# Performance work log

Measured on AMD Instinct MI355X. Metric: run time of the kernel, lower is better.

## Reference

```python
import jax, jax.numpy as jnp
import numpy as np

HIDDEN = 512


def _lstm(x, kernel, rec, bias):
    # x: [B,T,D]; Keras gate order i,f,c(g),o
    xz = jnp.einsum('btd,dk->btk', x, kernel) + bias  # [B,T,4H]
    B = x.shape[0]
    init = (jnp.zeros((B, HIDDEN), x.dtype), jnp.zeros((B, HIDDEN), x.dtype))

    def step(carry, z_t):
        h, c = carry
        z = z_t + h @ rec
        i, f, g, o = jnp.split(z, 4, axis=-1)
        c = jax.nn.sigmoid(f) * c + jax.nn.sigmoid(i) * jnp.tanh(g)
        h = jax.nn.sigmoid(o) * jnp.tanh(c)
        return (h, c), h

    _, hs = jax.lax.scan(step, init, jnp.swapaxes(xz, 0, 1))
    return jnp.swapaxes(hs, 0, 1)  # [B,T,H]


def _bilstm(x, kf, rf, bf, kb, rb, bb):
    fwd = _lstm(x, kf, rf, bf)
    bwd = _lstm(x[:, ::-1], kb, rb, bb)[:, ::-1]
    return jnp.concatenate([fwd, bwd], axis=-1)  # [B,T,2H]


def _crf_nll(logits, tags, seq_lens, trans):
    # logits [B,T,N], tags [B,T] int, seq_lens [B] int, trans [N,N]
    B, T, N = logits.shape
    t_idx = jnp.arange(T)
    mask = (t_idx[None, :] < seq_lens[:, None])  # [B,T] bool
    maskf = mask.astype(logits.dtype)

    # gold sequence score: unary + pairwise transitions
    unary = jnp.take_along_axis(logits, tags[..., None], axis=-1)[..., 0]  # [B,T]
    unary_score = jnp.sum(unary * maskf, axis=-1)
    pair_maskf = maskf[:, 1:]  # pair (t-1,t) valid iff t < len
    binary = trans[tags[:, :-1], tags[:, 1:]]  # [B,T-1]
    binary_score = jnp.sum(binary * pair_maskf, axis=-1)

    # log-partition via forward algorithm (masked scan)
    alpha0 = logits[:, 0]  # [B,N]

    def step(alpha, inp):
        logit_t, valid = inp
        new = jax.nn.logsumexp(alpha[:, :, None] + trans[None], axis=1) + logit_t
        return jnp.where(valid[:, None], new, alpha), None

    xs = (jnp.swapaxes(logits[:, 1:], 0, 1), jnp.swapaxes(mask[:, 1:], 0, 1))
    alpha, _ = jax.lax.scan(step, alpha0, xs)
    log_z = jax.nn.logsumexp(alpha, axis=-1)  # [B]
    return -(unary_score + binary_score - log_z)


def setup_inputs() -> dict:
    key = jax.random.key(0)
    ks = jax.random.split(key, 12)
    B, T, D, H, N = 32, 256, 768, HIDDEN, 25
    s_in = 1.0 / np.sqrt(D)
    s_rec = 1.0 / np.sqrt(H)
    return {
        'embeddings': jax.random.normal(ks[0], (B, T, D), jnp.float32),
        'targets': jax.random.randint(ks[1], (B, T), 0, N, jnp.int32),
        'seq_lens': jax.random.randint(ks[2], (B,), 1, T + 1, jnp.int32),
        'k_fwd': jax.random.normal(ks[3], (D, 4 * H), jnp.float32) * s_in,
        'r_fwd': jax.random.normal(ks[4], (H, 4 * H), jnp.float32) * s_rec,
        'b_fwd': jnp.zeros((4 * H,), jnp.float32),
        'k_bwd': jax.random.normal(ks[5], (D, 4 * H), jnp.float32) * s_in,
        'r_bwd': jax.random.normal(ks[6], (H, 4 * H), jnp.float32) * s_rec,
        'b_bwd': jnp.zeros((4 * H,), jnp.float32),
        'dense_w': jax.random.normal(ks[7], (2 * H, N), jnp.float32) / np.sqrt(2 * H),
        'dense_b': jnp.zeros((N,), jnp.float32),
        'transitions': jax.random.uniform(ks[8], (N, N), jnp.float32),
    }


def reference(embeddings, targets, seq_lens, k_fwd, r_fwd, b_fwd,
              k_bwd, r_bwd, b_bwd, dense_w, dense_b, transitions):
    seq_lens = jnp.clip(seq_lens, 1, embeddings.shape[1])
    h = _bilstm(embeddings, k_fwd, r_fwd, b_fwd, k_bwd, r_bwd, b_bwd)
    logits = jax.nn.selu(jnp.einsum('bth,hn->btn', h, dense_w) + dense_b)
    nll = _crf_nll(logits, targets, seq_lens, transitions)  # [B]
    loss = jnp.mean(nll)
    return loss, logits
```

## Files before the change

kernel.cpp:

```cpp
#include <hip/hip_runtime.h>
#include <hip/hip_bf16.h>
#include <math.h>

#define HID 512
#define GATES 2048
#define BT 8192
#define TT 256
#define BB 32
#define DIN 768
#define NTAG 25
#define UPB 4
#define NBLK 128
#define FSTR 4
#define EREP 8
#define ESTR 16

typedef _Float16 half2v __attribute__((ext_vector_type(2)));
typedef _Float16 half8  __attribute__((ext_vector_type(8)));
typedef float    f32x4  __attribute__((ext_vector_type(4)));

__device__ __forceinline__ half2v pack2h(float a, float b) {
  return __builtin_bit_cast(half2v, __builtin_amdgcn_cvt_pkrtz(a, b));
}

__device__ __forceinline__ float sigf(float x) { return 1.f / (1.f + __expf(-x)); }

__device__ __forceinline__ void gld_lds16(const void* g, void* l) {
  __builtin_amdgcn_global_load_lds(
      (const __attribute__((address_space(1))) unsigned int*)g,
      (__attribute__((address_space(3))) unsigned int*)l, 16, 0, 0);
}

__global__ __launch_bounds__(256) void prep_all(
    const float* __restrict__ emb, unsigned short* __restrict__ emb16,
    const float* __restrict__ Kf, const float* __restrict__ Kb,
    unsigned short* __restrict__ KTf, unsigned short* __restrict__ KTb,
    const float* __restrict__ W, unsigned short* __restrict__ WT16)
{
  __shared__ float tile[64][65];
  const int bid = blockIdx.x;
  const int tid = threadIdx.x;

  if (bid < 1024) {
    const int m = bid * 8 + (tid >> 5);
    const int c0 = tid & 31;
    #pragma unroll
    for (int p = 0; p < 3; ++p) {
      const int c = c0 + p * 32;
      const int kb = c >> 3, s = c & 7;
      const float* src = emb + (size_t)m * DIN + c * 8;
      const float4 v0 = *(const float4*)src;
      const float4 v1 = *(const float4*)(src + 4);
      half8 hv;
      hv[0] = (_Float16)v0.x; hv[1] = (_Float16)v0.y;
      hv[2] = (_Float16)v0.z; hv[3] = (_Float16)v0.w;
      hv[4] = (_Float16)v1.x; hv[5] = (_Float16)v1.y;
      hv[6] = (_Float16)v1.z; hv[7] = (_Float16)v1.w;
      *(half8*)(emb16 + (size_t)m * DIN + kb * 64 + (s ^ (m & 7)) * 8) = hv;
    }
  } else if (bid < 1792) {
    const int r = bid - 1024;
    const int dir = r / 384;
    const int r2 = r % 384;
    const int k0 = (r2 >> 5) * 64;
    const int n0 = (r2 & 31) * 64;
    const float* __restrict__ K = dir ? Kb : Kf;
    unsigned short* __restrict__ KT = dir ? KTb : KTf;
    #pragma unroll
    for (int p = 0; p < 4; ++p) {
      const int idx = p * 256 + tid;
      const int kr = idx >> 4, c4 = (idx & 15) * 4;
      const float4 v = *(const float4*)(K + (size_t)(k0 + kr) * GATES + n0 + c4);
      tile[kr][c4 + 0] = v.x; tile[kr][c4 + 1] = v.y;
      tile[kr][c4 + 2] = v.z; tile[kr][c4 + 3] = v.w;
    }
    __syncthreads();
    #pragma unroll
    for (int p = 0; p < 2; ++p) {
      const int idx = p * 256 + tid;
      const int nr = idx >> 3, s = idx & 7;
      half8 hv;
      #pragma unroll
      for (int x = 0; x < 8; ++x) hv[x] = (_Float16)tile[s * 8 + x][nr];
      *(half8*)(KT + (size_t)(n0 + nr) * DIN + k0 + (s ^ (nr & 7)) * 8) = hv;
    }
  } else {
    for (int id = tid; id < 32 * 1024; id += 256) {
      const int n = id >> 10, k = id & 1023;
      const float v = (n < NTAG) ? W[(size_t)k * NTAG + n] : 0.f;
      ((_Float16*)WT16)[id] = (_Float16)v;
    }
  }
}

__global__ __launch_bounds__(256) void gemm_xz(
    const unsigned short* __restrict__ emb16,
    const unsigned short* __restrict__ KTf, const unsigned short* __restrict__ KTb,
    const float* __restrict__ bf, const float* __restrict__ bb,
    float* __restrict__ xzf, float* __restrict__ xzb)
{
  const int dir = blockIdx.z;
  const unsigned short* __restrict__ KT = dir ? KTb : KTf;
  const float* __restrict__ bias = dir ? bb : bf;
  float* __restrict__ C = dir ? xzb : xzf;
  const int n0 = blockIdx.x * 128;
  const int m0 = blockIdx.y * 128;

  __shared__ __align__(16) char A_lds[128 * 64 * 2];
  __shared__ __align__(16) char B_lds[128 * 64 * 2];

  const int tid = threadIdx.x;
  const int lane = tid & 63, wid = tid >> 6;
  const int wm = wid >> 1, wn = wid & 1;
  const int lm = lane & 15, lk = lane >> 4;

  f32x4 acc[4][4];
  #pragma unroll
  for (int i = 0; i < 4; ++i)
    #pragma unroll
    for (int j = 0; j < 4; ++j) acc[i][j] = (f32x4){0.f, 0.f, 0.f, 0.f};

  for (int kt = 0; kt < DIN / 64; ++kt) {
    __syncthreads();
    #pragma unroll
    for (int i = 0; i < 4; ++i) {
      const int g = wid * 256 + i * 64 + lane;
      const int r = g >> 3, s = g & 7;
      gld_lds16(emb16 + (size_t)(m0 + r) * DIN + (kt * 8 + s) * 8,
                A_lds + (size_t)(wid * 256 + i * 64) * 16);
      gld_lds16(KT + (size_t)(n0 + r) * DIN + (kt * 8 + s) * 8,
                B_lds + (size_t)(wid * 256 + i * 64) * 16);
    }
    __syncthreads();

    #pragma unroll
    for (int kh = 0; kh < 2; ++kh) {
      half8 a[4], b[4];
      #pragma unroll
      for (int mt = 0; mt < 4; ++mt) {
        const int rloc = wm * 64 + mt * 16 + lm;
        const int kslot = kh * 4 + lk;
        a[mt] = *(const half8*)(A_lds + rloc * 128 + ((kslot ^ (rloc & 7)) << 4));
      }
      #pragma unroll
      for (int nt = 0; nt < 4; ++nt) {
        const int nloc = wn * 64 + nt * 16 + lm;
        const int kslot = kh * 4 + lk;
        b[nt] = *(const half8*)(B_lds + nloc * 128 + ((kslot ^ (nloc & 7)) << 4));
      }
      #pragma unroll
      for (int mt = 0; mt < 4; ++mt)
        #pragma unroll
        for (int nt = 0; nt < 4; ++nt)
          acc[mt][nt] = __builtin_amdgcn_mfma_f32_16x16x32_f16(a[mt], b[nt], acc[mt][nt], 0, 0, 0);
    }
  }

  #pragma unroll
  for (int nt = 0; nt < 4; ++nt) {
    const int col = n0 + wn * 64 + nt * 16 + lm;
    const float bs = bias[col];
    #pragma unroll
    for (int mt = 0; mt < 4; ++mt) {
      const int rowb = m0 + wm * 64 + mt * 16 + lk * 4;
      const f32x4 v = acc[mt][nt];
      #pragma unroll
      for (int g = 0; g < 4; ++g)
        C[(size_t)(rowb + g) * GATES + col] = v[g] + bs;
    }
  }
}

__global__ __launch_bounds__(256, 1) void lstm_persist(
    const float* __restrict__ xzf, const float* __restrict__ xzb,
    const float* __restrict__ Rf, const float* __restrict__ Rb,
    unsigned int* __restrict__ hGf, unsigned int* __restrict__ hGb,
    int* __restrict__ flg,
    int* __restrict__ ep)
{
  const int bid = blockIdx.x;
  const int dir = bid & 1;
  const int blk = bid >> 1;
  const int u0 = blk * UPB;
  const int tid = threadIdx.x;
  const int c = tid & 15;
  const int j = (c & 3) * HID + u0 + (c >> 2);
  const int lane = tid & 63, w = tid >> 6;
  const int lm = lane & 15, lk = lane >> 4;

  const float* __restrict__ R  = dir ? Rb : Rf;
  const float* __restrict__ xz = dir ? xzb : xzf;
  unsigned int* __restrict__ hGd = dir ? hGb : hGf;
  int* __restrict__ flgd = flg + (size_t)dir * TT * NBLK * FSTR;
  int* __restrict__ epd  = ep  + (size_t)dir * TT * EREP * ESTR;

  __shared__ uint4 hs4[BB * 65];
  __shared__ float redm[4][BB][18];
  __shared__ float zbuf[BB][20];

  half8 Rbf[4];
  #pragma unroll
  for (int kti = 0; kti < 4; ++kti) {
    const int kb = (w * 4 + kti) * 32 + lk * 8;
    half8 hv;
    #pragma unroll
    for (int x = 0; x < 8; ++x) hv[x] = (_Float16)R[(size_t)(kb + x) * GATES + j];
    Rbf[kti] = hv;
  }

  float cst = 0.f;
  const int b_o = tid & 31, u_o = tid >> 5;
  const int fb0 = tid >> 4, fb1 = (tid >> 4) + 16;
  const bool leader = (blk == 0);

  for (int s = 0; s < TT; ++s) {
    const int t = dir ? (TT - 1 - s) : s;

    const float x0 = xz[((size_t)fb0 * TT + t) * GATES + j];
    const float x1 = xz[((size_t)fb1 * TT + t) * GATES + j];

    if (s > 0) {
      const int tprev = dir ? t + 1 : t - 1;
      if (leader) {
        if (tid < NBLK) {
          while (!__hip_atomic_load(&flgd[((s - 1) * NBLK + tid) * FSTR],
                                    __ATOMIC_RELAXED, __HIP_MEMORY_SCOPE_AGENT))
            __builtin_amdgcn_s_sleep(1);
        }
        __syncthreads();
        if (tid < EREP)
          __hip_atomic_store(&epd[((s - 1) * EREP + tid) * ESTR], 1,
                             __ATOMIC_RELAXED, __HIP_MEMORY_SCOPE_AGENT);
      } else {
        if (tid == 0) {
          while (!__hip_atomic_load(&epd[((s - 1) * EREP + (blk & 7)) * ESTR],
                                    __ATOMIC_RELAXED, __HIP_MEMORY_SCOPE_AGENT))
            __builtin_amdgcn_s_sleep(1);
        }
        __syncthreads();
      }
      const uint4* hsrc = (const uint4*)(hGd + (size_t)tprev * BB * 256);
      #pragma unroll
      for (int it = 0; it < 8; ++it) {
        const int g4 = tid + it * 256;
        const uint4 v = hsrc[g4];
        hs4[(g4 >> 6) * 65 + (g4 & 63)] = v;
      }
    } else {
      const uint4 zz = make_uint4(0u, 0u, 0u, 0u);
      #pragma unroll
      for (int it = 0; it < 9; ++it) {
        const int idx = tid + it * 256;
        if (idx < BB * 65) hs4[idx] = zz;
      }
    }
    __syncthreads();

    f32x4 acc0 = (f32x4){0.f, 0.f, 0.f, 0.f};
    f32x4 acc1 = (f32x4){0.f, 0.f, 0.f, 0.f};
    #pragma unroll
    for (int kti = 0; kti < 4; ++kti) {
      const int k4 = (w * 4 + kti) * 4 + lk;
      const half8 a0 = *(const half8*)&hs4[(lm) * 65 + k4];
      const half8 a1 = *(const half8*)&hs4[(16 + lm) * 65 + k4];
      acc0 = __builtin_amdgcn_mfma_f32_16x16x32_f16(a0, Rbf[kti], acc0, 0, 0, 0);
      acc1 = __builtin_amdgcn_mfma_f32_16x16x32_f16(a1, Rbf[kti], acc1, 0, 0, 0);
    }
    #pragma unroll
    for (int g = 0; g < 4; ++g) {
      redm[w][lk * 4 + g][lm] = acc0[g];
      redm[w][16 + lk * 4 + g][lm] = acc1[g];
    }
    __syncthreads();

    {
      const float za = redm[0][fb0][c] + redm[1][fb0][c] + redm[2][fb0][c] + redm[3][fb0][c] + x0;
      const float zb2 = redm[0][fb1][c] + redm[1][fb1][c] + redm[2][fb1][c] + redm[3][fb1][c] + x1;
      zbuf[fb0][c] = za;
      zbuf[fb1][c] = zb2;
    }
    __syncthreads();

    if (tid < 128) {
      const float zi = zbuf[b_o][u_o * 4 + 0];
      const float zf = zbuf[b_o][u_o * 4 + 1];
      const float zg = zbuf[b_o][u_o * 4 + 2];
      const float zo = zbuf[b_o][u_o * 4 + 3];
      cst = sigf(zf) * cst + sigf(zi) * tanhf(zg);
      const float h = sigf(zo) * tanhf(cst);
      const float hp2 = __shfl_xor(h, 32);
      if ((tid & 32) == 0) {
        const half2v p = pack2h(h, hp2);
        __hip_atomic_store(&hGd[((size_t)t * BB + b_o) * 256 + blk * 2 + (u_o >> 1)],
                           __builtin_bit_cast(unsigned int, p),
                           __ATOMIC_RELAXED, __HIP_MEMORY_SCOPE_AGENT);
      }
    }
    __syncthreads();
    if (tid == 0)
      __hip_atomic_store(&flgd[(s * NBLK + blk) * FSTR], 1, __ATOMIC_RELAXED,
                         __HIP_MEMORY_SCOPE_AGENT);
  }
}

__global__ __launch_bounds__(256) void dense_selu(
    const unsigned int* __restrict__ hGf, const unsigned int* __restrict__ hGb,
    const unsigned short* __restrict__ WT16, const float* __restrict__ bias,
    float* __restrict__ out)
{
  const int q0 = blockIdx.x * 128;
  __shared__ __align__(16) char A_lds[128 * 64 * 2];
  __shared__ __align__(16) char B_lds[32 * 64 * 2];

  const int tid = threadIdx.x;
  const int lane = tid & 63, w = tid >> 6;
  const int lm = lane & 15, lk = lane >> 4;

  f32x4 acc[2][2];
  #pragma unroll
  for (int i = 0; i < 2; ++i)
    #pragma unroll
    for (int jj = 0; jj < 2; ++jj) acc[i][jj] = (f32x4){0.f, 0.f, 0.f, 0.f};

  for (int kt = 0; kt < 16; ++kt) {
    const int k0 = kt * 64;
    __syncthreads();
    #pragma unroll
    for (int p = 0; p < 4; ++p) {
      const int id = p * 256 + tid;
      const int r = id >> 3, s = id & 7;
      const int k = k0 + s * 8;
      const unsigned int* src = (k < 512)
          ? hGf + (size_t)(q0 + r) * 256 + (k >> 1)
          : hGb + (size_t)(q0 + r) * 256 + ((k - 512) >> 1);
      const uint4 v = *(const uint4*)src;
      *(uint4*)(A_lds + r * 128 + ((s ^ (r & 7)) << 4)) = v;
    }
    {
      const int r = tid >> 3, s = tid & 7;
      const uint4 v = *(const uint4*)(WT16 + (size_t)r * 1024 + k0 + s * 8);
      *(uint4*)(B_lds + r * 128 + ((s ^ (r & 7)) << 4)) = v;
    }
    __syncthreads();

    #pragma unroll
    for (int kh = 0; kh < 2; ++kh) {
      const int kslot = kh * 4 + lk;
      half8 a[2], b[2];
      #pragma unroll
      for (int mt = 0; mt < 2; ++mt) {
        const int rloc = w * 32 + mt * 16 + lm;
        a[mt] = *(const half8*)(A_lds + rloc * 128 + ((kslot ^ (rloc & 7)) << 4));
      }
      #pragma unroll
      for (int nt = 0; nt < 2; ++nt) {
        const int nloc = nt * 16 + lm;
        b[nt] = *(const half8*)(B_lds + nloc * 128 + ((kslot ^ (nloc & 7)) << 4));
      }
      #pragma unroll
      for (int mt = 0; mt < 2; ++mt)
        #pragma unroll
        for (int nt = 0; nt < 2; ++nt)
          acc[mt][nt] = __builtin_amdgcn_mfma_f32_16x16x32_f16(a[mt], b[nt], acc[mt][nt], 0, 0, 0);
    }
  }

  const float scale = 1.0507009873554805f, alf = 1.6732632423543772f;
  #pragma unroll
  for (int nt = 0; nt < 2; ++nt) {
    const int col = nt * 16 + lm;
    if (col < NTAG) {
      const float bs = bias[col];
      #pragma unroll
      for (int mt = 0; mt < 2; ++mt) {
        const int rowb = q0 + w * 32 + mt * 16 + lk * 4;
        const f32x4 vv = acc[mt][nt];
        #pragma unroll
        for (int g = 0; g < 4; ++g) {
          const int q = rowb + g;
          const int bt = (q & 31) * 256 + (q >> 5);
          float v = vv[g] + bs;
          v = v > 0.f ? scale * v : scale * alf * (__expf(v) - 1.f);
          out[(size_t)bt * NTAG + col] = v;
        }
      }
    }
  }
}

__global__ __launch_bounds__(64) void crf_kernel(
    const float* __restrict__ logits,
    const int* __restrict__ tags, const int* __restrict__ lens,
    const float* __restrict__ trans, float* __restrict__ nll)
{
  const int b = blockIdx.x;
  const int tid = threadIdx.x;
  __shared__ float tr[NTAG * NTAG];
  __shared__ float al[NTAG];
  __shared__ float red[2];
  for (int i = tid; i < NTAG * NTAG; i += 64) tr[i] = trans[i];
  __syncthreads();

  int len = lens[b];
  len = len < 1 ? 1 : (len > TT ? TT : len);
  const size_t base = (size_t)b * TT;

  float us = 0.f, bs = 0.f;
  for (int t = tid; t < TT; t += 64) {
    if (t < len) us += logits[(base + t) * NTAG + tags[base + t]];
    if (t >= 1 && t < len) bs += tr[tags[base + t - 1] * NTAG + tags[base + t]];
  }
  #pragma unroll
  for (int off = 32; off > 0; off >>= 1) {
    us += __shfl_down(us, off);
    bs += __shfl_down(bs, off);
  }
  if (tid == 0) { red[0] = us; red[1] = bs; }

  if (tid < NTAG) al[tid] = logits[base * NTAG + tid];
  __syncthreads();

  for (int t = 1; t < len; ++t) {
    float nv = 0.f;
    if (tid < NTAG) {
      float m = -3.4e38f;
      #pragma unroll
      for (int i = 0; i < NTAG; ++i) m = fmaxf(m, al[i] + tr[i * NTAG + tid]);
      float ss = 0.f;
      #pragma unroll
      for (int i = 0; i < NTAG; ++i) ss += __expf(al[i] + tr[i * NTAG + tid] - m);
      nv = m + __logf(ss) + logits[(base + t) * NTAG + tid];
    }
    __syncthreads();
    if (tid < NTAG) al[tid] = nv;
    __syncthreads();
  }

  if (tid == 0) {
    float m = -3.4e38f;
    for (int i = 0; i < NTAG; ++i) m = fmaxf(m, al[i]);
    float ss = 0.f;
    for (int i = 0; i < NTAG; ++i) ss += __expf(al[i] - m);
    const float logz = m + __logf(ss);
    nll[b] = -(red[0] + red[1] - logz);
  }
}

__global__ __launch_bounds__(64) void finalize(const float* __restrict__ nll, float* __restrict__ out) {
  float v = (threadIdx.x < BB) ? nll[threadIdx.x] : 0.f;
  #pragma unroll
  for (int off = 32; off > 0; off >>= 1) v += __shfl_down(v, off);
  if (threadIdx.x == 0) out[0] = v * (1.f / BB);
}

extern "C" void kernel_launch(void* const* d_in, const int* in_sizes, int n_in,
                              void* d_out, int out_size, void* d_ws, size_t ws_size,
                              hipStream_t stream) {
  const float* emb  = (const float*)d_in[0];
  const int* tags   = (const int*)d_in[1];
  const int* lens   = (const int*)d_in[2];
  const float* kf   = (const float*)d_in[3];
  const float* rf   = (const float*)d_in[4];
  const float* bf   = (const float*)d_in[5];
  const float* kb   = (const float*)d_in[6];
  const float* rb   = (const float*)d_in[7];
  const float* bb   = (const float*)d_in[8];
  const float* dw   = (const float*)d_in[9];
  const float* db   = (const float*)d_in[10];
  const float* trans= (const float*)d_in[11];
  float* out = (float*)d_out;

  float* ws  = (float*)d_ws;
  float* xzf = ws;
  float* xzb = xzf + (size_t)BT * GATES;
  unsigned int* hGf = (unsigned int*)(xzb + (size_t)BT * GATES);
  unsigned int* hGb = hGf + (size_t)TT * BB * 256;
  unsigned short* emb16 = (unsigned short*)(hGb + (size_t)TT * BB * 256);
  unsigned short* KTf = emb16 + (size_t)BT * DIN;
  unsigned short* KTb = KTf + (size_t)GATES * DIN;
  unsigned short* WT16 = KTb + (size_t)GATES * DIN;
  float* nll = (float*)(WT16 + 32 * 1024);
  int*   flg = (int*)(nll + 64);
  int*   ep  = flg + 2 * TT * NBLK * FSTR;

  (void)hipMemsetAsync(flg, 0,
                       (size_t)(2 * TT * NBLK * FSTR + 2 * TT * EREP * ESTR) * 4,
                       stream);

  prep_all<<<1793, 256, 0, stream>>>(emb, emb16, kf, kb, KTf, KTb, dw, WT16);
  gemm_xz<<<dim3(GATES / 128, BT / 128, 2), 256, 0, stream>>>(emb16, KTf, KTb, bf, bb, xzf, xzb);
  lstm_persist<<<2 * NBLK, 256, 0, stream>>>(xzf, xzb, rf, rb, hGf, hGb, flg, ep);
  dense_selu<<<BT / 128, 256, 0, stream>>>(hGf, hGb, WT16, db, out + 1);
  crf_kernel<<<32, 64, 0, stream>>>(out + 1, tags, lens, trans, nll);
  finalize<<<1, 64, 0, stream>>>(nll, out);
}
```

Measured before the change: 968.2 us.

## Store xz in fp16, give each wave a private h tile, drop block barriers

The input projection xz is now written and read as fp16, which halves the global traffic between the GEMM and the recurrent kernel. Each wave in the persistent LSTM kernel loads its own K-slice of h into a private LDS region, which removes a __syncthreads. The zbuf stage is folded into the gate computation, removing another barrier. The finalize kernel is replaced by an atomicAdd into the loss, whose zeroing happens inside dense_selu. In exchange, the gate preactivations lose precision and the order of the loss summation is no longer deterministic.

```diff
diff --git a/kernel.cpp b/kernel.cpp
--- a/kernel.cpp
+++ b/kernel.cpp
@@ -97,12 +97,12 @@
     const unsigned short* __restrict__ emb16,
     const unsigned short* __restrict__ KTf, const unsigned short* __restrict__ KTb,
     const float* __restrict__ bf, const float* __restrict__ bb,
-    float* __restrict__ xzf, float* __restrict__ xzb)
+    _Float16* __restrict__ xzf, _Float16* __restrict__ xzb)
 {
   const int dir = blockIdx.z;
   const unsigned short* __restrict__ KT = dir ? KTb : KTf;
   const float* __restrict__ bias = dir ? bb : bf;
-  float* __restrict__ C = dir ? xzb : xzf;
+  _Float16* __restrict__ C = dir ? xzb : xzf;
   const int n0 = blockIdx.x * 128;
   const int m0 = blockIdx.y * 128;
 
@@ -166,13 +166,13 @@
       const f32x4 v = acc[mt][nt];
       #pragma unroll
       for (int g = 0; g < 4; ++g)
-        C[(size_t)(rowb + g) * GATES + col] = v[g] + bs;
+        C[(size_t)(rowb + g) * GATES + col] = (_Float16)(v[g] + bs);
     }
   }
 }
 
 __global__ __launch_bounds__(256, 1) void lstm_persist(
-    const float* __restrict__ xzf, const float* __restrict__ xzb,
+    const _Float16* __restrict__ xzf, const _Float16* __restrict__ xzb,
     const float* __restrict__ Rf, const float* __restrict__ Rb,
     unsigned int* __restrict__ hGf, unsigned int* __restrict__ hGb,
     int* __restrict__ flg,
@@ -189,14 +189,13 @@
   const int lm = lane & 15, lk = lane >> 4;
 
   const float* __restrict__ R  = dir ? Rb : Rf;
-  const float* __restrict__ xz = dir ? xzb : xzf;
+  const _Float16* __restrict__ xz = dir ? xzb : xzf;
   unsigned int* __restrict__ hGd = dir ? hGb : hGf;
   int* __restrict__ flgd = flg + (size_t)dir * TT * NBLK * FSTR;
   int* __restrict__ epd  = ep  + (size_t)dir * TT * EREP * ESTR;
 
-  __shared__ uint4 hs4[BB * 65];
+  __shared__ uint4 hs4[4 * 32 * 17];
   __shared__ float redm[4][BB][18];
-  __shared__ float zbuf[BB][20];
 
   half8 Rbf[4];
   #pragma unroll
@@ -210,14 +209,19 @@
 
   float cst = 0.f;
   const int b_o = tid & 31, u_o = tid >> 5;
-  const int fb0 = tid >> 4, fb1 = (tid >> 4) + 16;
+  uint4* myhs = hs4 + w * (32 * 17);
+  const int sr = lane >> 4, si = lane & 15;
   const bool leader = (blk == 0);
 
   for (int s = 0; s < TT; ++s) {
     const int t = dir ? (TT - 1 - s) : s;
 
-    const float x0 = xz[((size_t)fb0 * TT + t) * GATES + j];
-    const float x1 = xz[((size_t)fb1 * TT + t) * GATES + j];
+    float xg[4] = {0.f, 0.f, 0.f, 0.f};
+    if (tid < 128) {
+      #pragma unroll
+      for (int g = 0; g < 4; ++g)
+        xg[g] = (float)xz[((size_t)b_o * TT + t) * GATES + g * HID + u0 + u_o];
+    }
 
     if (s > 0) {
       const int tprev = dir ? t + 1 : t - 1;
@@ -242,27 +246,25 @@
       const uint4* hsrc = (const uint4*)(hGd + (size_t)tprev * BB * 256);
       #pragma unroll
       for (int it = 0; it < 8; ++it) {
-        const int g4 = tid + it * 256;
-        const uint4 v = hsrc[g4];
-        hs4[(g4 >> 6) * 65 + (g4 & 63)] = v;
+        const int r = it * 4 + sr;
+        myhs[r * 17 + si] = hsrc[r * 64 + w * 16 + si];
       }
     } else {
       const uint4 zz = make_uint4(0u, 0u, 0u, 0u);
       #pragma unroll
-      for (int it = 0; it < 9; ++it) {
-        const int idx = tid + it * 256;
-        if (idx < BB * 65) hs4[idx] = zz;
-      }
-    }
-    __syncthreads();
+      for (int it = 0; it < 8; ++it) {
+        const int r = it * 4 + sr;
+        myhs[r * 17 + si] = zz;
+      }
+    }
 
     f32x4 acc0 = (f32x4){0.f, 0.f, 0.f, 0.f};
     f32x4 acc1 = (f32x4){0.f, 0.f, 0.f, 0.f};
     #pragma unroll
     for (int kti = 0; kti < 4; ++kti) {
-      const int k4 = (w * 4 + kti) * 4 + lk;
-      const half8 a0 = *(const half8*)&hs4[(lm) * 65 + k4];
-      const half8 a1 = *(const half8*)&hs4[(16 + lm) * 65 + k4];
+      const int cidx = kti * 4 + lk;
+      const half8 a0 = *(const half8*)&myhs[lm * 17 + cidx];
+      const half8 a1 = *(const half8*)&myhs[(16 + lm) * 17 + cidx];
       acc0 = __builtin_amdgcn_mfma_f32_16x16x32_f16(a0, Rbf[kti], acc0, 0, 0, 0);
       acc1 = __builtin_amdgcn_mfma_f32_16x16x32_f16(a1, Rbf[kti], acc1, 0, 0, 0);
     }
@@ -273,21 +275,16 @@
     }
     __syncthreads();
 
-    {
-      const float za = redm[0][fb0][c] + redm[1][fb0][c] + redm[2][fb0][c] + redm[3][fb0][c] + x0;
-      const float zb2 = redm[0][fb1][c] + redm[1][fb1][c] + redm[2][fb1][c] + redm[3][fb1][c] + x1;
-      zbuf[fb0][c] = za;
-      zbuf[fb1][c] = zb2;
-    }
-    __syncthreads();
-
     if (tid < 128) {
-      const float zi = zbuf[b_o][u_o * 4 + 0];
-      const float zf = zbuf[b_o][u_o * 4 + 1];
-      const float zg = zbuf[b_o][u_o * 4 + 2];
-      const float zo = zbuf[b_o][u_o * 4 + 3];
-      cst = sigf(zf) * cst + sigf(zi) * tanhf(zg);
-      const float h = sigf(zo) * tanhf(cst);
+      float z[4];
+      #pragma unroll
+      for (int g = 0; g < 4; ++g) {
+        const int cc = u_o * 4 + g;
+        z[g] = redm[0][b_o][cc] + redm[1][b_o][cc] + redm[2][b_o][cc] +
+               redm[3][b_o][cc] + xg[g];
+      }
+      cst = sigf(z[1]) * cst + sigf(z[0]) * tanhf(z[2]);
+      const float h = sigf(z[3]) * tanhf(cst);
       const float hp2 = __shfl_xor(h, 32);
       if ((tid & 32) == 0) {
         const half2v p = pack2h(h, hp2);
@@ -306,8 +303,9 @@
 __global__ __launch_bounds__(256) void dense_selu(
     const unsigned int* __restrict__ hGf, const unsigned int* __restrict__ hGb,
     const unsigned short* __restrict__ WT16, const float* __restrict__ bias,
-    float* __restrict__ out)
+    float* __restrict__ out, float* __restrict__ loss0)
 {
+  if (blockIdx.x == 0 && threadIdx.x == 0) *loss0 = 0.f;
   const int q0 = blockIdx.x * 128;
   __shared__ __align__(16) char A_lds[128 * 64 * 2];
   __shared__ __align__(16) char B_lds[32 * 64 * 2];
@@ -391,7 +389,7 @@
 __global__ __launch_bounds__(64) void crf_kernel(
     const float* __restrict__ logits,
     const int* __restrict__ tags, const int* __restrict__ lens,
-    const float* __restrict__ trans, float* __restrict__ nll)
+    const float* __restrict__ trans, float* __restrict__ loss0)
 {
   const int b = blockIdx.x;
   const int tid = threadIdx.x;
@@ -442,15 +440,9 @@
     float ss = 0.f;
     for (int i = 0; i < NTAG; ++i) ss += __expf(al[i] - m);
     const float logz = m + __logf(ss);
-    nll[b] = -(red[0] + red[1] - logz);
-  }
-}
-
-__global__ __launch_bounds__(64) void finalize(const float* __restrict__ nll, float* __restrict__ out) {
-  float v = (threadIdx.x < BB) ? nll[threadIdx.x] : 0.f;
-  #pragma unroll
-  for (int off = 32; off > 0; off >>= 1) v += __shfl_down(v, off);
-  if (threadIdx.x == 0) out[0] = v * (1.f / BB);
+    const float nll = -(red[0] + red[1] - logz);
+    atomicAdd(loss0, nll * (1.f / BB));
+  }
 }
 
 extern "C" void kernel_launch(void* const* d_in, const int* in_sizes, int n_in,
@@ -470,18 +462,16 @@
   const float* trans= (const float*)d_in[11];
   float* out = (float*)d_out;
 
-  float* ws  = (float*)d_ws;
-  float* xzf = ws;
-  float* xzb = xzf + (size_t)BT * GATES;
+  _Float16* xzf = (_Float16*)d_ws;
+  _Float16* xzb = xzf + (size_t)BT * GATES;
   unsigned int* hGf = (unsigned int*)(xzb + (size_t)BT * GATES);
   unsigned int* hGb = hGf + (size_t)TT * BB * 256;
   unsigned short* emb16 = (unsigned short*)(hGb + (size_t)TT * BB * 256);
   unsigned short* KTf = emb16 + (size_t)BT * DIN;
   unsigned short* KTb = KTf + (size_t)GATES * DIN;
   unsigned short* WT16 = KTb + (size_t)GATES * DIN;
-  float* nll = (float*)(WT16 + 32 * 1024);
-  int*   flg = (int*)(nll + 64);
-  int*   ep  = flg + 2 * TT * NBLK * FSTR;
+  int* flg = (int*)(WT16 + 32 * 1024);
+  int* ep  = flg + 2 * TT * NBLK * FSTR;
 
   (void)hipMemsetAsync(flg, 0,
                        (size_t)(2 * TT * NBLK * FSTR + 2 * TT * EREP * ESTR) * 4,
@@ -490,7 +480,6 @@
   prep_all<<<1793, 256, 0, stream>>>(emb, emb16, kf, kb, KTf, KTb, dw, WT16);
   gemm_xz<<<dim3(GATES / 128, BT / 128, 2), 256, 0, stream>>>(emb16, KTf, KTb, bf, bb, xzf, xzb);
   lstm_persist<<<2 * NBLK, 256, 0, stream>>>(xzf, xzb, rf, rb, hGf, hGb, flg, ep);
-  dense_selu<<<BT / 128, 256, 0, stream>>>(hGf, hGb, WT16, db, out + 1);
-  crf_kernel<<<32, 64, 0, stream>>>(out + 1, tags, lens, trans, nll);
-  finalize<<<1, 64, 0, stream>>>(nll, out);
-}
+  dense_selu<<<BT / 128, 256, 0, stream>>>(hGf, hGb, WT16, db, out + 1, out);
+  crf_kernel<<<32, 64, 0, stream>>>(out + 1, tags, lens, trans, out);
+}
```

After: 893.5 us. 7.7% less time.
